# Performance work log

Hardware: AMD Instinct MI355X
Metric: run time of the kernel (lower is better)

Reference implementation:

```python
import math
import jax, jax.numpy as jnp
import numpy as np

ALPHA = 0.2  # LeakyReLU negative slope
MASK_VAL = -9e15


def _positional_encoding(n: int, d: int) -> jnp.ndarray:
    # Custom PE with a (1 + exp(-pos/100)) decay factor, matching CustomPositionalEncoding
    position = jnp.arange(n, dtype=jnp.float32)[:, None]            # [N,1]
    div_term = jnp.exp(jnp.arange(0, d, 2, dtype=jnp.float32) * (-math.log(10000.0) / d))
    decay = 1.0 + jnp.exp(-position / 100.0)                         # [N,1]
    pe = jnp.zeros((n, d), dtype=jnp.float32)
    pe = pe.at[:, 0::2].set(jnp.sin(position * div_term) * decay)
    pe = pe.at[:, 1::2].set(jnp.cos(position * div_term) * decay)
    return pe[None]                                                  # [1,N,d]


def setup_inputs() -> dict:
    key = jax.random.key(0)
    k_h, k_adj, k_W, k_a = jax.random.split(key, 4)
    B, N, IN_F, OUT_F = 8, 2048, 128, 128
    h = jax.random.normal(k_h, (B, N, IN_F), dtype=jnp.float32)
    # sparse-ish 0/1 adjacency (float, as in the torch module)
    adj = jax.random.randint(k_adj, (B, N, N), 0, 2).astype(jnp.float32)
    # xavier_uniform init scale
    limW = math.sqrt(6.0 / (IN_F + OUT_F))
    W = jax.random.uniform(k_W, (IN_F, OUT_F), minval=-limW, maxval=limW, dtype=jnp.float32)
    lima = math.sqrt(6.0 / (2 * OUT_F + 1))
    a = jax.random.uniform(k_a, (2 * OUT_F, 1), minval=-lima, maxval=lima, dtype=jnp.float32)
    return {"h": h, "adj": adj, "W": W, "a": a}


def reference(h, adj, W, a):
    B, N, _ = h.shape
    out_f = W.shape[1]
    h = h + _positional_encoding(N, h.shape[2])
    # force self-loops
    eye = jnp.eye(N, dtype=adj.dtype)[None]
    adj = jnp.where(eye > 0, jnp.ones_like(adj), adj)
    Wh = jnp.einsum('bni,io->bno', h, W)                 # [B,N,out_f]
    a1 = a[:out_f, 0]
    a2 = a[out_f:, 0]
    s1 = Wh @ a1                                          # [B,N]
    s2 = Wh @ a2                                          # [B,N]
    e = s1[:, :, None] + s2[:, None, :]                   # [B,N,N] additive score
    e = jnp.where(e >= 0, e, ALPHA * e)                   # leaky relu
    attn = jnp.where(adj > 0, e, MASK_VAL)
    attn = jax.nn.softmax(attn, axis=-1)
    # dropout is identity in eval mode
    h_prime = jnp.einsum('bnm,bmo->bno', attn, Wh)        # [B,N,out_f]
    deg = adj.sum(-1)                                     # [B,N]
    valid = deg > 0
    valid = valid.at[:, 0].set(False)
    denom = jnp.clip(valid.sum(1, keepdims=True), 1, None).astype(h_prime.dtype)  # [B,1]
    g = (h_prime * valid[:, :, None]).sum(1) / denom      # [B,out_f] masked mean pool
    return jax.nn.elu(g)
```

## Files before the change

kernel.cpp:

```cpp
#include <hip/hip_runtime.h>
#include <math.h>

#define NN 2048
#define BATCH 8
#define FDIM 128

__global__ void k_pe(float* __restrict__ pe) {
    int i = blockIdx.x * 256 + threadIdx.x;
    int n = i >> 7;
    int k = i & 127;
    int jj = k >> 1;
    float dt = expf((float)(2 * jj) * (-0.07195578415606394f));
    float ang = (float)n * dt;
    float decay = 1.f + expf(-(float)n * 0.01f);
    float v = ((k & 1) == 0 ? sinf(ang) : cosf(ang)) * decay;
    pe[i] = v;
}

__global__ __launch_bounds__(512) void k_wh(const float* __restrict__ h,
                                            const float* __restrict__ pe,
                                            const float* __restrict__ W,
                                            const float* __restrict__ a,
                                            float* __restrict__ Wh,
                                            float* __restrict__ s1,
                                            float* __restrict__ s2) {
    __shared__ float w_lds[64 * 128];
    __shared__ float hpe_lds[64 * 68];
    const int b  = blockIdx.y;
    const int n0 = blockIdx.x * 64;
    const int t  = threadIdx.x;
    const int tc = t & 15;
    const int tr = t >> 4;

    float acc[2][8];
#pragma unroll
    for (int i = 0; i < 2; i++)
#pragma unroll
        for (int j = 0; j < 8; j++) acc[i][j] = 0.f;

    for (int kp = 0; kp < 2; ++kp) {
        {
            const float4* wsrc = (const float4*)(W + kp * 64 * 128);
            float4* wdst = (float4*)w_lds;
#pragma unroll
            for (int q = 0; q < 4; q++) wdst[t + q * 512] = wsrc[t + q * 512];
        }
        {
#pragma unroll
            for (int q = 0; q < 2; q++) {
                int f = t + q * 512;
                int r = f >> 4;
                int k4 = (f & 15) << 2;
                int n = n0 + r;
                int kk = kp * 64 + k4;
                float4 hv = *(const float4*)(h + ((size_t)b * NN + n) * FDIM + kk);
                float4 pv = *(const float4*)(pe + (size_t)n * FDIM + kk);
                *(float4*)(hpe_lds + r * 68 + k4) =
                    make_float4(hv.x + pv.x, hv.y + pv.y, hv.z + pv.z, hv.w + pv.w);
            }
        }
        __syncthreads();
#pragma unroll 4
        for (int k = 0; k < 64; k++) {
            float wv[8];
            float4 wa = *(float4*)(w_lds + k * 128 + tc * 8);
            float4 wb = *(float4*)(w_lds + k * 128 + tc * 8 + 4);
            wv[0] = wa.x; wv[1] = wa.y; wv[2] = wa.z; wv[3] = wa.w;
            wv[4] = wb.x; wv[5] = wb.y; wv[6] = wb.z; wv[7] = wb.w;
#pragma unroll
            for (int i = 0; i < 2; i++) {
                float hv = hpe_lds[(tr * 2 + i) * 68 + k];
#pragma unroll
                for (int j = 0; j < 8; j++) acc[i][j] = fmaf(hv, wv[j], acc[i][j]);
            }
        }
        __syncthreads();
    }

    float a1v[8], a2v[8];
#pragma unroll
    for (int j = 0; j < 8; j++) { a1v[j] = a[tc * 8 + j]; a2v[j] = a[FDIM + tc * 8 + j]; }
#pragma unroll
    for (int i = 0; i < 2; i++) {
        int n = n0 + tr * 2 + i;
        float* dst = Wh + ((size_t)b * NN + n) * FDIM + tc * 8;
        *(float4*)dst = make_float4(acc[i][0], acc[i][1], acc[i][2], acc[i][3]);
        *(float4*)(dst + 4) = make_float4(acc[i][4], acc[i][5], acc[i][6], acc[i][7]);
        float p1 = 0.f, p2 = 0.f;
#pragma unroll
        for (int j = 0; j < 8; j++) {
            p1 = fmaf(acc[i][j], a1v[j], p1);
            p2 = fmaf(acc[i][j], a2v[j], p2);
        }
#pragma unroll
        for (int off = 1; off < 16; off <<= 1) {
            p1 += __shfl_xor(p1, off, 64);
            p2 += __shfl_xor(p2, off, 64);
        }
        if (tc == 0) {
            s1[(size_t)b * NN + n] = p1;
            s2[(size_t)b * NN + n] = p2;
        }
    }
}

__global__ __launch_bounds__(256) void k_attn(const float* __restrict__ adj,
                                              const float* __restrict__ s1,
                                              const float* __restrict__ s2,
                                              float* __restrict__ c_part) {
    const int b = blockIdx.y;
    const int chunk = blockIdx.x;
    const int t = threadIdx.x;
    const int wave = t >> 6;
    const int lane = t & 63;
    __shared__ float c_lds[NN];
    for (int i = t; i < NN; i += 256) c_lds[i] = 0.f;
    __syncthreads();

    const float* s2b = s2 + (size_t)b * NN;
    float s2v[32];
#pragma unroll
    for (int kq = 0; kq < 8; kq++) {
        float4 v = *(const float4*)(s2b + kq * 256 + lane * 4);
        s2v[kq * 4 + 0] = v.x; s2v[kq * 4 + 1] = v.y;
        s2v[kq * 4 + 2] = v.z; s2v[kq * 4 + 3] = v.w;
    }
    float c_acc[32];
#pragma unroll
    for (int j = 0; j < 32; j++) c_acc[j] = 0.f;

    const int nbase = chunk * 16;
    const float* adjb = adj + (size_t)b * NN * NN;
    const float* s1b = s1 + (size_t)b * NN;

#pragma unroll 1
    for (int ri = 0; ri < 4; ri++) {
        int n = nbase + wave * 4 + ri;
        if (n == 0) continue;
        float s1n = s1b[n];
        const float* arow = adjb + (size_t)n * NN;
        unsigned mask = 0u;
        float zsum = 0.f;
#pragma unroll
        for (int kq = 0; kq < 8; kq++) {
            float4 av = *(const float4*)(arow + kq * 256 + lane * 4);
            float a4[4] = {av.x, av.y, av.z, av.w};
#pragma unroll
            for (int e = 0; e < 4; e++) {
                int j = kq * 4 + e;
                int m = kq * 256 + lane * 4 + e;
                float x = s1n + s2v[j];
                float ev = fmaxf(x, 0.2f * x);
                bool conn = (a4[e] > 0.f) || (m == n);
                mask |= (unsigned)conn << j;
                zsum += conn ? __expf(ev) : 0.f;
            }
        }
#pragma unroll
        for (int off = 32; off; off >>= 1) zsum += __shfl_xor(zsum, off, 64);
        float rz = 1.f / zsum;
#pragma unroll
        for (int kq = 0; kq < 8; kq++)
#pragma unroll
            for (int e = 0; e < 4; e++) {
                int j = kq * 4 + e;
                float x = s1n + s2v[j];
                float ev = fmaxf(x, 0.2f * x);
                float p = ((mask >> j) & 1u) ? __expf(ev) : 0.f;
                c_acc[j] = fmaf(p, rz, c_acc[j]);
            }
    }

#pragma unroll
    for (int kq = 0; kq < 8; kq++)
#pragma unroll
        for (int e = 0; e < 4; e++)
            atomicAdd(&c_lds[kq * 256 + lane * 4 + e], c_acc[kq * 4 + e]);
    __syncthreads();

    float* dst = c_part + ((size_t)b * 128 + chunk) * NN;
#pragma unroll
    for (int q = 0; q < 2; q++) {
        int idx = t + q * 256;
        ((float4*)dst)[idx] = ((const float4*)c_lds)[idx];
    }
}

__global__ __launch_bounds__(256) void k_gpre(const float* __restrict__ Wh,
                                              const float* __restrict__ c_part,
                                              float* __restrict__ g_part) {
    const int b = blockIdx.y;
    const int mc = blockIdx.x;
    const int m0 = mc * 64;
    const int t = threadIdx.x;
    __shared__ float red[256];
    __shared__ float c_lds[64];

    {
        const int mi = t & 63;
        const int w = t >> 6;
        const float* cp = c_part + (size_t)b * 128 * NN + m0 + mi;
        float s = 0.f;
#pragma unroll 8
        for (int j = 0; j < 32; j++) s += cp[(size_t)(w * 32 + j) * NN];
        red[w * 64 + mi] = s;
    }
    __syncthreads();
    if (t < 64) c_lds[t] = red[t] + red[t + 64] + red[t + 128] + red[t + 192];
    __syncthreads();

    const int o = t & 127;
    const int mh = t >> 7;
    float acc = 0.f;
    const float* whb = Wh + ((size_t)b * NN + m0 + mh * 32) * FDIM;
#pragma unroll 4
    for (int mm = 0; mm < 32; mm++)
        acc = fmaf(c_lds[mh * 32 + mm], whb[mm * FDIM + o], acc);
    g_part[((size_t)(mc * 2 + mh)) * (BATCH * FDIM) + b * FDIM + o] = acc;
}

__global__ void k_elu(const float* __restrict__ g_part, float* __restrict__ out) {
    int i = blockIdx.x * 256 + threadIdx.x;
    if (i < BATCH * FDIM) {
        float s = 0.f;
#pragma unroll 8
        for (int p = 0; p < 64; p++) s += g_part[p * (BATCH * FDIM) + i];
        float g = s * (1.0f / 2047.0f);
        out[i] = g > 0.f ? g : expm1f(g);
    }
}

extern "C" void kernel_launch(void* const* d_in, const int* in_sizes, int n_in,
                              void* d_out, int out_size, void* d_ws, size_t ws_size,
                              hipStream_t stream) {
    (void)in_sizes; (void)n_in; (void)out_size; (void)ws_size;
    const float* h   = (const float*)d_in[0];
    const float* adj = (const float*)d_in[1];
    const float* W   = (const float*)d_in[2];
    const float* a   = (const float*)d_in[3];
    float* out = (float*)d_out;

    char* ws = (char*)d_ws;
    float* Wh     = (float*)ws;
    float* pe     = Wh + (size_t)BATCH * NN * FDIM;
    float* s1     = pe + (size_t)NN * FDIM;
    float* s2     = s1 + (size_t)BATCH * NN;
    float* c_part = s2 + (size_t)BATCH * NN;
    float* g_part = c_part + (size_t)BATCH * 128 * NN;

    hipLaunchKernelGGL(k_pe, dim3(NN * FDIM / 256), dim3(256), 0, stream, pe);
    hipLaunchKernelGGL(k_wh, dim3(NN / 64, BATCH), dim3(512), 0, stream,
                       h, pe, W, a, Wh, s1, s2);
    hipLaunchKernelGGL(k_attn, dim3(NN / 16, BATCH), dim3(256), 0, stream,
                       adj, s1, s2, c_part);
    hipLaunchKernelGGL(k_gpre, dim3(NN / 64, BATCH), dim3(256), 0, stream,
                       Wh, c_part, g_part);
    hipLaunchKernelGGL(k_elu, dim3(4), dim3(256), 0, stream, g_part, out);
}
```

Before: 259.6 us.

## Process two adjacency rows per wave with all loads issued upfront

The attention kernel now gives each wave two rows instead of four sequential ones. All sixteen float4 adjacency loads for both rows are issued before any compute, and exponentials are computed once and kept in registers rather than recomputed in a second pass. s2 is staged in shared memory instead of registers. The grid doubles to 256 chunks per batch, so the c_part buffer and the k_gpre reduction grow twofold, adding partial-sum traffic and more LDS atomics per row.

```diff
diff --git a/kernel.cpp b/kernel.cpp
--- a/kernel.cpp
+++ b/kernel.cpp
@@ -114,71 +114,72 @@
     const int wave = t >> 6;
     const int lane = t & 63;
     __shared__ float c_lds[NN];
+    __shared__ float s2_lds[NN];
+    const float* s2b = s2 + (size_t)b * NN;
     for (int i = t; i < NN; i += 256) c_lds[i] = 0.f;
-    __syncthreads();
-
-    const float* s2b = s2 + (size_t)b * NN;
-    float s2v[32];
-#pragma unroll
-    for (int kq = 0; kq < 8; kq++) {
-        float4 v = *(const float4*)(s2b + kq * 256 + lane * 4);
-        s2v[kq * 4 + 0] = v.x; s2v[kq * 4 + 1] = v.y;
-        s2v[kq * 4 + 2] = v.z; s2v[kq * 4 + 3] = v.w;
-    }
-    float c_acc[32];
-#pragma unroll
-    for (int j = 0; j < 32; j++) c_acc[j] = 0.f;
-
-    const int nbase = chunk * 16;
+#pragma unroll
+    for (int q = 0; q < 2; q++) {
+        int idx = t + q * 256;
+        ((float4*)s2_lds)[idx] = ((const float4*)s2b)[idx];
+    }
+    __syncthreads();
+
+    const int na = chunk * 8 + wave * 2;
+    const int nb_ = na + 1;
     const float* adjb = adj + (size_t)b * NN * NN;
     const float* s1b = s1 + (size_t)b * NN;
-
-#pragma unroll 1
-    for (int ri = 0; ri < 4; ri++) {
-        int n = nbase + wave * 4 + ri;
-        if (n == 0) continue;
-        float s1n = s1b[n];
-        const float* arow = adjb + (size_t)n * NN;
-        unsigned mask = 0u;
-        float zsum = 0.f;
-#pragma unroll
-        for (int kq = 0; kq < 8; kq++) {
-            float4 av = *(const float4*)(arow + kq * 256 + lane * 4);
-            float a4[4] = {av.x, av.y, av.z, av.w};
-#pragma unroll
-            for (int e = 0; e < 4; e++) {
-                int j = kq * 4 + e;
-                int m = kq * 256 + lane * 4 + e;
-                float x = s1n + s2v[j];
-                float ev = fmaxf(x, 0.2f * x);
-                bool conn = (a4[e] > 0.f) || (m == n);
-                mask |= (unsigned)conn << j;
-                zsum += conn ? __expf(ev) : 0.f;
-            }
-        }
-#pragma unroll
-        for (int off = 32; off; off >>= 1) zsum += __shfl_xor(zsum, off, 64);
-        float rz = 1.f / zsum;
-#pragma unroll
-        for (int kq = 0; kq < 8; kq++)
-#pragma unroll
-            for (int e = 0; e < 4; e++) {
-                int j = kq * 4 + e;
-                float x = s1n + s2v[j];
-                float ev = fmaxf(x, 0.2f * x);
-                float p = ((mask >> j) & 1u) ? __expf(ev) : 0.f;
-                c_acc[j] = fmaf(p, rz, c_acc[j]);
-            }
-    }
+    const float s1A = s1b[na];
+    const float s1B = s1b[nb_];
+    const float4* rowA = (const float4*)(adjb + (size_t)na * NN);
+    const float4* rowB = (const float4*)(adjb + (size_t)nb_ * NN);
+
+    float4 avA[8], avB[8];
+#pragma unroll
+    for (int kq = 0; kq < 8; kq++) avA[kq] = rowA[kq * 64 + lane];
+#pragma unroll
+    for (int kq = 0; kq < 8; kq++) avB[kq] = rowB[kq * 64 + lane];
+
+    float pA[32], pB[32];
+    float zA = 0.f, zB = 0.f;
+#pragma unroll
+    for (int kq = 0; kq < 8; kq++) {
+        float4 sv = ((const float4*)s2_lds)[kq * 64 + lane];
+        float sv4[4] = {sv.x, sv.y, sv.z, sv.w};
+        float aA[4] = {avA[kq].x, avA[kq].y, avA[kq].z, avA[kq].w};
+        float aB[4] = {avB[kq].x, avB[kq].y, avB[kq].z, avB[kq].w};
+#pragma unroll
+        for (int e = 0; e < 4; e++) {
+            int j = kq * 4 + e;
+            int m = kq * 256 + lane * 4 + e;
+            float xA = s1A + sv4[e];
+            float evA = fmaxf(xA, 0.2f * xA);
+            float vA = ((aA[e] > 0.f) || (m == na)) ? __expf(evA) : 0.f;
+            pA[j] = vA; zA += vA;
+            float xB = s1B + sv4[e];
+            float evB = fmaxf(xB, 0.2f * xB);
+            float vB = ((aB[e] > 0.f) || (m == nb_)) ? __expf(evB) : 0.f;
+            pB[j] = vB; zB += vB;
+        }
+    }
+#pragma unroll
+    for (int off = 32; off; off >>= 1) {
+        zA += __shfl_xor(zA, off, 64);
+        zB += __shfl_xor(zB, off, 64);
+    }
+    const float rzA = (na != 0) ? 1.f / zA : 0.f;
+    const float rzB = 1.f / zB;
 
 #pragma unroll
     for (int kq = 0; kq < 8; kq++)
 #pragma unroll
-        for (int e = 0; e < 4; e++)
-            atomicAdd(&c_lds[kq * 256 + lane * 4 + e], c_acc[kq * 4 + e]);
-    __syncthreads();
-
-    float* dst = c_part + ((size_t)b * 128 + chunk) * NN;
+        for (int e = 0; e < 4; e++) {
+            int j = kq * 4 + e;
+            int m = kq * 256 + lane * 4 + e;
+            atomicAdd(&c_lds[m], pA[j] * rzA + pB[j] * rzB);
+        }
+    __syncthreads();
+
+    float* dst = c_part + ((size_t)b * 256 + chunk) * NN;
 #pragma unroll
     for (int q = 0; q < 2; q++) {
         int idx = t + q * 256;
@@ -199,10 +200,10 @@
     {
         const int mi = t & 63;
         const int w = t >> 6;
-        const float* cp = c_part + (size_t)b * 128 * NN + m0 + mi;
+        const float* cp = c_part + (size_t)b * 256 * NN + m0 + mi;
         float s = 0.f;
 #pragma unroll 8
-        for (int j = 0; j < 32; j++) s += cp[(size_t)(w * 32 + j) * NN];
+        for (int j = 0; j < 64; j++) s += cp[(size_t)(w * 64 + j) * NN];
         red[w * 64 + mi] = s;
     }
     __syncthreads();
@@ -246,12 +247,12 @@
     float* s1     = pe + (size_t)NN * FDIM;
     float* s2     = s1 + (size_t)BATCH * NN;
     float* c_part = s2 + (size_t)BATCH * NN;
-    float* g_part = c_part + (size_t)BATCH * 128 * NN;
+    float* g_part = c_part + (size_t)BATCH * 256 * NN;
 
     hipLaunchKernelGGL(k_pe, dim3(NN * FDIM / 256), dim3(256), 0, stream, pe);
     hipLaunchKernelGGL(k_wh, dim3(NN / 64, BATCH), dim3(512), 0, stream,
                        h, pe, W, a, Wh, s1, s2);
-    hipLaunchKernelGGL(k_attn, dim3(NN / 16, BATCH), dim3(256), 0, stream,
+    hipLaunchKernelGGL(k_attn, dim3(NN / 8, BATCH), dim3(256), 0, stream,
                        adj, s1, s2, c_part);
     hipLaunchKernelGGL(k_gpre, dim3(NN / 64, BATCH), dim3(256), 0, stream,
                        Wh, c_part, g_part);
```

Result: slower. 303.3 us (+16.8%).

## Prefetch next adjacency row and use per-wave LDS slices in attention kernel

Applied to the files above, without the earlier changes.

The attention kernel now double-buffers adjacency rows in registers, loading row n+1 while row n is processed. Each row's exponentials are computed once and kept, rather than recomputed in a second pass. The s2 scores move from registers into LDS, and shared atomics are replaced by per-wave LDS accumulation slices summed at the end. This targets global load latency, redundant exp work and LDS atomic contention, at the cost of more registers and about 40KB of LDS per block (launch_bounds 256,1).

```diff
diff --git a/kernel.cpp b/kernel.cpp
--- a/kernel.cpp
+++ b/kernel.cpp
@@ -104,85 +104,100 @@
     }
 }
 
-__global__ __launch_bounds__(256) void k_attn(const float* __restrict__ adj,
-                                              const float* __restrict__ s1,
-                                              const float* __restrict__ s2,
-                                              float* __restrict__ c_part) {
+__global__ __launch_bounds__(256, 1) void k_attn(const float* __restrict__ adj,
+                                                 const float* __restrict__ s1,
+                                                 const float* __restrict__ s2,
+                                                 float* __restrict__ c_part) {
     const int b = blockIdx.y;
     const int chunk = blockIdx.x;
     const int t = threadIdx.x;
     const int wave = t >> 6;
     const int lane = t & 63;
-    __shared__ float c_lds[NN];
-    for (int i = t; i < NN; i += 256) c_lds[i] = 0.f;
-    __syncthreads();
+    __shared__ float s2_lds[NN];
+    __shared__ float slice[4][NN];
 
     const float* s2b = s2 + (size_t)b * NN;
-    float s2v[32];
-#pragma unroll
-    for (int kq = 0; kq < 8; kq++) {
-        float4 v = *(const float4*)(s2b + kq * 256 + lane * 4);
-        s2v[kq * 4 + 0] = v.x; s2v[kq * 4 + 1] = v.y;
-        s2v[kq * 4 + 2] = v.z; s2v[kq * 4 + 3] = v.w;
-    }
-    float c_acc[32];
-#pragma unroll
-    for (int j = 0; j < 32; j++) c_acc[j] = 0.f;
-
-    const int nbase = chunk * 16;
+#pragma unroll
+    for (int q = 0; q < 2; q++) {
+        int idx = t + q * 256;
+        ((float4*)s2_lds)[idx] = ((const float4*)s2b)[idx];
+    }
+#pragma unroll
+    for (int kq = 0; kq < 8; kq++)
+        *(float4*)&slice[wave][kq * 256 + lane * 4] = make_float4(0.f, 0.f, 0.f, 0.f);
+    __syncthreads();
+
+    const int nbase = chunk * 16 + wave * 4;
     const float* adjb = adj + (size_t)b * NN * NN;
     const float* s1b = s1 + (size_t)b * NN;
 
-#pragma unroll 1
+    float4 cur[8], nxt[8];
+    {
+        const float4* rp = (const float4*)(adjb + (size_t)nbase * NN);
+#pragma unroll
+        for (int kq = 0; kq < 8; kq++) cur[kq] = rp[kq * 64 + lane];
+    }
+
+#pragma unroll
     for (int ri = 0; ri < 4; ri++) {
-        int n = nbase + wave * 4 + ri;
-        if (n == 0) continue;
-        float s1n = s1b[n];
-        const float* arow = adjb + (size_t)n * NN;
-        unsigned mask = 0u;
-        float zsum = 0.f;
+        const int n = nbase + ri;
+        if (ri < 3) {
+            const float4* rq = (const float4*)(adjb + (size_t)(n + 1) * NN);
+#pragma unroll
+            for (int kq = 0; kq < 8; kq++) nxt[kq] = rq[kq * 64 + lane];
+        }
+        const float s1n = s1b[n];
+        float p[32];
+        float z = 0.f;
 #pragma unroll
         for (int kq = 0; kq < 8; kq++) {
-            float4 av = *(const float4*)(arow + kq * 256 + lane * 4);
+            float4 av = cur[kq];
+            float4 sv = ((const float4*)s2_lds)[kq * 64 + lane];
             float a4[4] = {av.x, av.y, av.z, av.w};
+            float s4[4] = {sv.x, sv.y, sv.z, sv.w};
 #pragma unroll
             for (int e = 0; e < 4; e++) {
                 int j = kq * 4 + e;
                 int m = kq * 256 + lane * 4 + e;
-                float x = s1n + s2v[j];
+                float x = s1n + s4[e];
                 float ev = fmaxf(x, 0.2f * x);
                 bool conn = (a4[e] > 0.f) || (m == n);
-                mask |= (unsigned)conn << j;
-                zsum += conn ? __expf(ev) : 0.f;
+                float pe_ = conn ? __expf(ev) : 0.f;
+                p[j] = pe_;
+                z += pe_;
             }
         }
 #pragma unroll
-        for (int off = 32; off; off >>= 1) zsum += __shfl_xor(zsum, off, 64);
-        float rz = 1.f / zsum;
-#pragma unroll
-        for (int kq = 0; kq < 8; kq++)
-#pragma unroll
-            for (int e = 0; e < 4; e++) {
-                int j = kq * 4 + e;
-                float x = s1n + s2v[j];
-                float ev = fmaxf(x, 0.2f * x);
-                float p = ((mask >> j) & 1u) ? __expf(ev) : 0.f;
-                c_acc[j] = fmaf(p, rz, c_acc[j]);
-            }
-    }
-
-#pragma unroll
-    for (int kq = 0; kq < 8; kq++)
-#pragma unroll
-        for (int e = 0; e < 4; e++)
-            atomicAdd(&c_lds[kq * 256 + lane * 4 + e], c_acc[kq * 4 + e]);
+        for (int off = 32; off; off >>= 1) z += __shfl_xor(z, off, 64);
+        const float rz = (n != 0) ? 1.f / z : 0.f;
+#pragma unroll
+        for (int kq = 0; kq < 8; kq++) {
+            float4 cv = *(float4*)&slice[wave][kq * 256 + lane * 4];
+            cv.x += p[kq * 4 + 0] * rz;
+            cv.y += p[kq * 4 + 1] * rz;
+            cv.z += p[kq * 4 + 2] * rz;
+            cv.w += p[kq * 4 + 3] * rz;
+            *(float4*)&slice[wave][kq * 256 + lane * 4] = cv;
+        }
+        if (ri < 3) {
+#pragma unroll
+            for (int kq = 0; kq < 8; kq++) cur[kq] = nxt[kq];
+        }
+    }
     __syncthreads();
 
     float* dst = c_part + ((size_t)b * 128 + chunk) * NN;
 #pragma unroll
     for (int q = 0; q < 2; q++) {
         int idx = t + q * 256;
-        ((float4*)dst)[idx] = ((const float4*)c_lds)[idx];
+        float4 v0 = ((const float4*)slice[0])[idx];
+        float4 v1 = ((const float4*)slice[1])[idx];
+        float4 v2 = ((const float4*)slice[2])[idx];
+        float4 v3 = ((const float4*)slice[3])[idx];
+        ((float4*)dst)[idx] = make_float4(v0.x + v1.x + v2.x + v3.x,
+                                          v0.y + v1.y + v2.y + v3.y,
+                                          v0.z + v1.z + v2.z + v3.z,
+                                          v0.w + v1.w + v2.w + v3.w);
     }
 }
 
```

Result: faster. 222.7 us (-14.2%).

## Pack adjacency into bitmask, fuse positional encoding, drop LDS atomics in attention

Applied to the files above, without the earlier changes.

A new streaming kernel converts the float adjacency matrix into a 32-bit-per-word bitmask with the self-loop bits already set. The attention kernel then reads that compact mask instead of the float rows, which separates bulk memory streaming from the exp-heavy compute. The positional encoding is now computed inline in the Wh GEMM loader, removing the separate PE kernel and its buffer. Per-column LDS atomicAdds are replaced by per-wave shared slices that are summed at write-out. The trade-offs are an extra kernel launch, a mask buffer in the workspace, recomputed sin/cos/exp in the GEMM loader, and four times more LDS in the attention kernel.

```diff
diff --git a/kernel.cpp b/kernel.cpp
--- a/kernel.cpp
+++ b/kernel.cpp
@@ -4,21 +4,28 @@
 #define NN 2048
 #define BATCH 8
 #define FDIM 128
-
-__global__ void k_pe(float* __restrict__ pe) {
-    int i = blockIdx.x * 256 + threadIdx.x;
-    int n = i >> 7;
-    int k = i & 127;
-    int jj = k >> 1;
-    float dt = expf((float)(2 * jj) * (-0.07195578415606394f));
-    float ang = (float)n * dt;
-    float decay = 1.f + expf(-(float)n * 0.01f);
-    float v = ((k & 1) == 0 ? sinf(ang) : cosf(ang)) * decay;
-    pe[i] = v;
+#define NWORDS (BATCH * NN * 64)
+
+__global__ __launch_bounds__(256) void k_conv(const float* __restrict__ adj,
+                                              unsigned* __restrict__ mask) {
+    const int g = blockIdx.x * 256 + threadIdx.x;
+    const float4* src = (const float4*)(adj + (size_t)g * 32);
+    unsigned w = 0u;
+#pragma unroll
+    for (int i = 0; i < 8; i++) {
+        float4 v = src[i];
+        w |= (v.x > 0.f ? 1u : 0u) << (i * 4 + 0);
+        w |= (v.y > 0.f ? 1u : 0u) << (i * 4 + 1);
+        w |= (v.z > 0.f ? 1u : 0u) << (i * 4 + 2);
+        w |= (v.w > 0.f ? 1u : 0u) << (i * 4 + 3);
+    }
+    const int n = (g >> 6) & (NN - 1);
+    const int wordIdx = g & 63;
+    if (wordIdx == (n >> 5)) w |= 1u << (n & 31);
+    mask[g] = w;
 }
 
 __global__ __launch_bounds__(512) void k_wh(const float* __restrict__ h,
-                                            const float* __restrict__ pe,
                                             const float* __restrict__ W,
                                             const float* __restrict__ a,
                                             float* __restrict__ Wh,
@@ -31,6 +38,7 @@
     const int t  = threadIdx.x;
     const int tc = t & 15;
     const int tr = t >> 4;
+    const float C2 = -0.07195578415606394f;
 
     float acc[2][8];
 #pragma unroll
@@ -54,9 +62,16 @@
                 int n = n0 + r;
                 int kk = kp * 64 + k4;
                 float4 hv = *(const float4*)(h + ((size_t)b * NN + n) * FDIM + kk);
-                float4 pv = *(const float4*)(pe + (size_t)n * FDIM + kk);
-                *(float4*)(hpe_lds + r * 68 + k4) =
-                    make_float4(hv.x + pv.x, hv.y + pv.y, hv.z + pv.z, hv.w + pv.w);
+                float fn = (float)n;
+                float decay = 1.f + expf(-fn * 0.01f);
+                float dt0 = expf((float)kk * C2);
+                float dt1 = expf((float)(kk + 2) * C2);
+                float ang0 = fn * dt0, ang1 = fn * dt1;
+                hv.x += sinf(ang0) * decay;
+                hv.y += cosf(ang0) * decay;
+                hv.z += sinf(ang1) * decay;
+                hv.w += cosf(ang1) * decay;
+                *(float4*)(hpe_lds + r * 68 + k4) = hv;
             }
         }
         __syncthreads();
@@ -104,24 +119,22 @@
     }
 }
 
-__global__ __launch_bounds__(256) void k_attn(const float* __restrict__ adj,
-                                              const float* __restrict__ s1,
-                                              const float* __restrict__ s2,
-                                              float* __restrict__ c_part) {
+__global__ __launch_bounds__(256, 4) void k_attn(const unsigned* __restrict__ mask,
+                                                 const float* __restrict__ s1,
+                                                 const float* __restrict__ s2,
+                                                 float* __restrict__ c_part) {
     const int b = blockIdx.y;
     const int chunk = blockIdx.x;
     const int t = threadIdx.x;
     const int wave = t >> 6;
     const int lane = t & 63;
-    __shared__ float c_lds[NN];
-    for (int i = t; i < NN; i += 256) c_lds[i] = 0.f;
-    __syncthreads();
+    __shared__ float slice[4][NN];
 
     const float* s2b = s2 + (size_t)b * NN;
     float s2v[32];
 #pragma unroll
     for (int kq = 0; kq < 8; kq++) {
-        float4 v = *(const float4*)(s2b + kq * 256 + lane * 4);
+        float4 v = ((const float4*)s2b)[kq * 64 + lane];
         s2v[kq * 4 + 0] = v.x; s2v[kq * 4 + 1] = v.y;
         s2v[kq * 4 + 2] = v.z; s2v[kq * 4 + 3] = v.w;
     }
@@ -129,60 +142,60 @@
 #pragma unroll
     for (int j = 0; j < 32; j++) c_acc[j] = 0.f;
 
-    const int nbase = chunk * 16;
-    const float* adjb = adj + (size_t)b * NN * NN;
+    const int nbase = chunk * 16 + wave * 4;
     const float* s1b = s1 + (size_t)b * NN;
+    const unsigned sh = (lane & 7) << 2;
 
 #pragma unroll 1
     for (int ri = 0; ri < 4; ri++) {
-        int n = nbase + wave * 4 + ri;
-        if (n == 0) continue;
-        float s1n = s1b[n];
-        const float* arow = adjb + (size_t)n * NN;
-        unsigned mask = 0u;
-        float zsum = 0.f;
-#pragma unroll
-        for (int kq = 0; kq < 8; kq++) {
-            float4 av = *(const float4*)(arow + kq * 256 + lane * 4);
-            float a4[4] = {av.x, av.y, av.z, av.w};
+        const int n = nbase + ri;
+        const unsigned* mrow = mask + ((size_t)b * NN + n) * 64;
+        const float s1n = s1b[n];
+        unsigned mw[8];
+#pragma unroll
+        for (int kq = 0; kq < 8; kq++) mw[kq] = mrow[kq * 8 + (lane >> 3)];
+        float z = 0.f;
+#pragma unroll
+        for (int kq = 0; kq < 8; kq++)
 #pragma unroll
             for (int e = 0; e < 4; e++) {
-                int j = kq * 4 + e;
-                int m = kq * 256 + lane * 4 + e;
-                float x = s1n + s2v[j];
+                float x = s1n + s2v[kq * 4 + e];
                 float ev = fmaxf(x, 0.2f * x);
-                bool conn = (a4[e] > 0.f) || (m == n);
-                mask |= (unsigned)conn << j;
-                zsum += conn ? __expf(ev) : 0.f;
-            }
-        }
-#pragma unroll
-        for (int off = 32; off; off >>= 1) zsum += __shfl_xor(zsum, off, 64);
-        float rz = 1.f / zsum;
+                z += ((mw[kq] >> (sh + e)) & 1u) ? __expf(ev) : 0.f;
+            }
+#pragma unroll
+        for (int off = 32; off; off >>= 1) z += __shfl_xor(z, off, 64);
+        const float rz = (n != 0) ? 1.f / z : 0.f;
 #pragma unroll
         for (int kq = 0; kq < 8; kq++)
 #pragma unroll
             for (int e = 0; e < 4; e++) {
-                int j = kq * 4 + e;
-                float x = s1n + s2v[j];
+                float x = s1n + s2v[kq * 4 + e];
                 float ev = fmaxf(x, 0.2f * x);
-                float p = ((mask >> j) & 1u) ? __expf(ev) : 0.f;
-                c_acc[j] = fmaf(p, rz, c_acc[j]);
+                float p = ((mw[kq] >> (sh + e)) & 1u) ? __expf(ev) : 0.f;
+                c_acc[kq * 4 + e] = fmaf(p, rz, c_acc[kq * 4 + e]);
             }
     }
 
 #pragma unroll
     for (int kq = 0; kq < 8; kq++)
-#pragma unroll
-        for (int e = 0; e < 4; e++)
-            atomicAdd(&c_lds[kq * 256 + lane * 4 + e], c_acc[kq * 4 + e]);
+        *(float4*)&slice[wave][kq * 256 + lane * 4] =
+            make_float4(c_acc[kq * 4 + 0], c_acc[kq * 4 + 1],
+                        c_acc[kq * 4 + 2], c_acc[kq * 4 + 3]);
     __syncthreads();
 
     float* dst = c_part + ((size_t)b * 128 + chunk) * NN;
 #pragma unroll
     for (int q = 0; q < 2; q++) {
         int idx = t + q * 256;
-        ((float4*)dst)[idx] = ((const float4*)c_lds)[idx];
+        float4 v0 = ((const float4*)slice[0])[idx];
+        float4 v1 = ((const float4*)slice[1])[idx];
+        float4 v2 = ((const float4*)slice[2])[idx];
+        float4 v3 = ((const float4*)slice[3])[idx];
+        ((float4*)dst)[idx] = make_float4(v0.x + v1.x + v2.x + v3.x,
+                                          v0.y + v1.y + v2.y + v3.y,
+                                          v0.z + v1.z + v2.z + v3.z,
+                                          v0.w + v1.w + v2.w + v3.w);
     }
 }
 
@@ -241,18 +254,19 @@
     float* out = (float*)d_out;
 
     char* ws = (char*)d_ws;
-    float* Wh     = (float*)ws;
-    float* pe     = Wh + (size_t)BATCH * NN * FDIM;
-    float* s1     = pe + (size_t)NN * FDIM;
-    float* s2     = s1 + (size_t)BATCH * NN;
-    float* c_part = s2 + (size_t)BATCH * NN;
-    float* g_part = c_part + (size_t)BATCH * 128 * NN;
-
-    hipLaunchKernelGGL(k_pe, dim3(NN * FDIM / 256), dim3(256), 0, stream, pe);
+    float* Wh       = (float*)ws;
+    float* s1       = Wh + (size_t)BATCH * NN * FDIM;
+    float* s2       = s1 + (size_t)BATCH * NN;
+    float* c_part   = s2 + (size_t)BATCH * NN;
+    float* g_part   = c_part + (size_t)BATCH * 128 * NN;
+    unsigned* mask  = (unsigned*)(g_part + 64 * BATCH * FDIM);
+
+    hipLaunchKernelGGL(k_conv, dim3(NWORDS / 256), dim3(256), 0, stream,
+                       adj, mask);
     hipLaunchKernelGGL(k_wh, dim3(NN / 64, BATCH), dim3(512), 0, stream,
-                       h, pe, W, a, Wh, s1, s2);
+                       h, W, a, Wh, s1, s2);
     hipLaunchKernelGGL(k_attn, dim3(NN / 16, BATCH), dim3(256), 0, stream,
-                       adj, s1, s2, c_part);
+                       mask, s1, s2, c_part);
     hipLaunchKernelGGL(k_gpre, dim3(NN / 64, BATCH), dim3(256), 0, stream,
                        Wh, c_part, g_part);
     hipLaunchKernelGGL(k_elu, dim3(4), dim3(256), 0, stream, g_part, out);
```

After: 234.1 us. -9.8%, faster.
